# Performance work log

Measured on AMD Instinct MI355X. Metric: run time of the kernel, lower is better.

Reference implementation:

```python
import jax, jax.numpy as jnp
import numpy as np

U_NODES, V_NODES, N_EDGES = 100000, 50000, 2000000
F_DIM, G_DIM, H_DIM = 32, 32, 8
G_HIDDEN = (64, 32)
F_HIDDEN = (64, 32)
OUT_DIM = 1


def _linear_params(key, din, dout):
    kw, kb = jax.random.split(key)
    lim = 1.0 / np.sqrt(din)
    w = jax.random.uniform(kw, (din, dout), jnp.float32, -lim, lim)
    b = jax.random.uniform(kb, (dout,), jnp.float32, -lim, lim)
    return w, b


def setup_inputs() -> dict:
    key = jax.random.key(0)
    ks = jax.random.split(key, 10)
    u = jax.random.normal(ks[0], (U_NODES, F_DIM), jnp.float32)
    v = jax.random.normal(ks[1], (V_NODES, G_DIM), jnp.float32)
    e_vals = jax.random.normal(ks[2], (N_EDGES, H_DIM), jnp.float32)
    e_src = jax.random.randint(ks[3], (N_EDGES,), 0, V_NODES, jnp.int32)  # V-side index (indices[0])
    e_dst = jax.random.randint(ks[4], (N_EDGES,), 0, U_NODES, jnp.int32)  # U-side index (indices[1])
    g_w1, g_b1 = _linear_params(ks[5], F_DIM + G_DIM + H_DIM, G_HIDDEN[0])
    g_w2, g_b2 = _linear_params(ks[6], G_HIDDEN[0], G_HIDDEN[1])
    f_w1, f_b1 = _linear_params(ks[7], F_DIM + G_HIDDEN[1], F_HIDDEN[0])
    f_w2, f_b2 = _linear_params(ks[8], F_HIDDEN[0], F_HIDDEN[1])
    t_w, t_b = _linear_params(ks[9], F_HIDDEN[1], OUT_DIM)
    return {
        "u": u, "v": v, "e_vals": e_vals, "e_src": e_src, "e_dst": e_dst,
        "g_w1": g_w1, "g_b1": g_b1, "g_w2": g_w2, "g_b2": g_b2,
        "f_w1": f_w1, "f_b1": f_b1, "f_w2": f_w2, "f_b2": f_b2,
        "t_w": t_w, "t_b": t_b,
    }


def reference(u, v, e_vals, e_src, e_dst,
              g_w1, g_b1, g_w2, g_b2,
              f_w1, f_b1, f_w2, f_b2,
              t_w, t_b):
    # gather edge endpoint features -> g MLP (two Linear+ReLU layers)
    edge_in = jnp.concatenate([u[e_dst], v[e_src], e_vals], axis=-1)  # (E, F+G+H)
    h = jax.nn.relu(edge_in @ g_w1 + g_b1)
    h = jax.nn.relu(h @ g_w2 + g_b2)  # (E, D)
    # torch.sparse.sum over dim=-3 (V axis) == segment-sum by the U index
    agg = jax.ops.segment_sum(h, e_dst, num_segments=u.shape[0])  # (U, D)
    # f MLP on concat([u, agg])
    z = jax.nn.relu(jnp.concatenate([u, agg], axis=-1) @ f_w1 + f_b1)
    z = jax.nn.relu(z @ f_w2 + f_b2)
    # tail linear (no relu) + sigmoid
    return jax.nn.sigmoid(z @ t_w + t_b)  # (U, 1)
```

## Files before the change

kernel.cpp:

```cpp
#include <hip/hip_runtime.h>
#include <cstdint>
#include <cstddef>

#define U_NODES 100000
#define V_NODES 50000
#define N_EDGES 2000000


typedef _Float16 f16x8 __attribute__((ext_vector_type(8)));
typedef _Float16 f16x2 __attribute__((ext_vector_type(2)));
typedef float    f32x4 __attribute__((ext_vector_type(4)));

__device__ __forceinline__ void load8f(const float* __restrict__ p, float* x) {
    const float4* p4 = reinterpret_cast<const float4*>(p);
    float4 a = p4[0], b = p4[1];
    x[0]=a.x; x[1]=a.y; x[2]=a.z; x[3]=a.w;
    x[4]=b.x; x[5]=b.y; x[6]=b.z; x[7]=b.w;
}

__device__ __forceinline__ void load32f(const float* __restrict__ p, float* x) {
    #pragma unroll
    for (int q = 0; q < 4; ++q) load8f(p + 8*q, x + 8*q);
}

__device__ __forceinline__ unsigned pack_bf16x2(float a, float b) {
    unsigned ua = __float_as_uint(a);
    ua = (ua + 0x7FFFu + ((ua >> 16) & 1u)) >> 16;
    unsigned ub = __float_as_uint(b);
    ub = (ub + 0x7FFFu + ((ub >> 16) & 1u)) & 0xFFFF0000u;
    return ua | ub;
}
__device__ __forceinline__ unsigned short bf16_1(float a) {
    unsigned ua = __float_as_uint(a);
    return (unsigned short)((ua + 0x7FFFu + ((ua >> 16) & 1u)) >> 16);
}

__device__ __forceinline__ unsigned pk16(float a, float b) {
    union { f16x2 h; unsigned u; } c;
    c.h[0] = (_Float16)a; c.h[1] = (_Float16)b;
    return c.u;
}
__device__ __forceinline__ float f16lo(unsigned w) {
    union { unsigned short u; _Float16 h; } c; c.u = (unsigned short)(w & 0xFFFFu);
    return (float)c.h;
}
__device__ __forceinline__ float f16hi(unsigned w) {
    union { unsigned short u; _Float16 h; } c; c.u = (unsigned short)(w >> 16);
    return (float)c.h;
}
__device__ __forceinline__ f16x8 as_f16x8(uint4 x) {
    union { uint4 u; f16x8 h; } c; c.u = x; return c.h;
}

__device__ __forceinline__ float fdot2f(unsigned a, unsigned b, float c) {
#if defined(__has_builtin) && __has_builtin(__builtin_amdgcn_fdot2)
    union { unsigned u; f16x2 h; } ca, cb; ca.u = a; cb.u = b;
    return __builtin_amdgcn_fdot2(ca.h, cb.h, c, false);
#else
    return c + f16lo(a)*f16lo(b) + f16hi(a)*f16hi(b);
#endif
}


__global__ __launch_bounds__(256) void proj_u_kernel(
    const float* __restrict__ u, const float* __restrict__ g_w1,
    float* __restrict__ A)
{
    int n = blockIdx.x * 256 + threadIdx.x;
    if (n >= U_NODES) return;
    float x[32];
    load32f(u + (size_t)n * 32, x);
    float acc[64];
    #pragma unroll
    for (int j = 0; j < 64; ++j) acc[j] = 0.f;
    #pragma unroll
    for (int i = 0; i < 32; ++i) {
        #pragma unroll
        for (int j = 0; j < 64; ++j) acc[j] += x[i] * g_w1[i*64 + j];
    }
    float4* Ap = reinterpret_cast<float4*>(A + (size_t)n * 64);
    #pragma unroll
    for (int q = 0; q < 16; ++q)
        Ap[q] = make_float4(acc[4*q], acc[4*q+1], acc[4*q+2], acc[4*q+3]);
}

__global__ __launch_bounds__(256) void proj_v_kernel(
    const float* __restrict__ v, const float* __restrict__ g_w1,
    const float* __restrict__ g_b1, float* __restrict__ B)
{
    int n = blockIdx.x * 256 + threadIdx.x;
    if (n >= V_NODES) return;
    float x[32];
    load32f(v + (size_t)n * 32, x);
    float acc[64];
    #pragma unroll
    for (int j = 0; j < 64; ++j) acc[j] = g_b1[j];
    #pragma unroll
    for (int i = 0; i < 32; ++i) {
        #pragma unroll
        for (int j = 0; j < 64; ++j) acc[j] += x[i] * g_w1[(32+i)*64 + j];
    }
    float4* Bp = reinterpret_cast<float4*>(B + (size_t)n * 64);
    #pragma unroll
    for (int q = 0; q < 16; ++q)
        Bp[q] = make_float4(acc[4*q], acc[4*q+1], acc[4*q+2], acc[4*q+3]);
}


__global__ __launch_bounds__(256) void rank_kernel(
    const int* __restrict__ e_dst, int* __restrict__ deg, int* __restrict__ rank)
{
    int e = blockIdx.x * 256 + threadIdx.x;
    if (e >= N_EDGES) return;
    rank[e] = atomicAdd(&deg[e_dst[e]], 1);
}

__global__ __launch_bounds__(256) void scan_block_kernel(
    const int* __restrict__ deg, int* __restrict__ off, int* __restrict__ aux, int n)
{
    __shared__ int s[256];
    int tid = threadIdx.x;
    int i = blockIdx.x * 256 + tid;
    int x = (i < n) ? deg[i] : 0;
    s[tid] = x;
    __syncthreads();
    #pragma unroll
    for (int o = 1; o < 256; o <<= 1) {
        int t = (tid >= o) ? s[tid - o] : 0;
        __syncthreads();
        s[tid] += t;
        __syncthreads();
    }
    if (i < n) off[i + 1] = s[tid];
    if (tid == 255) aux[blockIdx.x] = s[255];
}

__global__ __launch_bounds__(512) void scan_aux_kernel(int* __restrict__ aux, int nA)
{
    __shared__ int s[512];
    int tid = threadIdx.x;
    int x = (tid < nA) ? aux[tid] : 0;
    s[tid] = x;
    __syncthreads();
    #pragma unroll
    for (int o = 1; o < 512; o <<= 1) {
        int t = (tid >= o) ? s[tid - o] : 0;
        __syncthreads();
        s[tid] += t;
        __syncthreads();
    }
    if (tid < nA) aux[tid] = s[tid] - x;
}

__global__ __launch_bounds__(256) void scan_add_kernel(
    int* __restrict__ off, const int* __restrict__ aux, int n)
{
    int i = blockIdx.x * 256 + threadIdx.x;
    if (i == 0) off[0] = 0;
    if (i < n) off[i + 1] += aux[i >> 8];
}

__global__ __launch_bounds__(256) void scatter_kernel(
    const int* __restrict__ e_dst, const int* __restrict__ off,
    const int* __restrict__ rank, int* __restrict__ sorted_eid)
{
    int e = blockIdx.x * 256 + threadIdx.x;
    if (e >= N_EDGES) return;
    int d = e_dst[e];
    sorted_eid[off[d] + rank[e]] = e;
}

__global__ __launch_bounds__(256) void permute_pack_kernel(
    const int* __restrict__ e_dst, const int* __restrict__ e_src,
    const int* __restrict__ rank, const int* __restrict__ off,
    const float* __restrict__ e_vals, unsigned* __restrict__ epk)
{
    int e = blockIdx.x * 256 + threadIdx.x;
    if (e >= N_EDGES) return;
    int d = e_dst[e];
    int pos = off[d] + rank[e];
    float ev[8];
    load8f(e_vals + (size_t)e * 8, ev);
    uint4 w0;
    w0.x = (unsigned)d;
    w0.y = (unsigned)e_src[e];
    w0.z = pk16(ev[0], ev[1]);
    w0.w = pk16(ev[2], ev[3]);
    uint2 w1;
    w1.x = pk16(ev[4], ev[5]);
    w1.y = pk16(ev[6], ev[7]);
    unsigned* dst = epk + (size_t)pos * 8;
    *reinterpret_cast<uint4*>(dst)     = w0;
    *reinterpret_cast<uint2*>(dst + 4) = w1;
}


__global__ __launch_bounds__(256) void edge_frag_kernel(
    const float* __restrict__ A, const float* __restrict__ B,
    const unsigned* __restrict__ epk,
    const float* __restrict__ g_w1, const float* __restrict__ g_w2,
    const float* __restrict__ g_b2, float* __restrict__ agg)
{
    __shared__ unsigned s_w2[32 * 33];
    __shared__ __align__(16) unsigned s_w1e[4 * 64];
    __shared__ unsigned s_h2[256 * 17];
    __shared__ int s_d[256];
    __shared__ int s_heads[256];
    __shared__ int s_cnt, s_prevd, s_nextd;

    const int tid = threadIdx.x;
    const long bP = (long)blockIdx.x * 256;

    #pragma unroll
    for (int i = 0; i < 4; ++i) {
        int idx = tid + i * 256;
        int kp = idx >> 5, n = idx & 31;
        s_w2[kp * 33 + n] = pk16(g_w2[(2*kp)*32 + n], g_w2[(2*kp+1)*32 + n]);
    }
    {
        int i2 = tid >> 6, c = tid & 63;
        s_w1e[i2 * 64 + c] = pk16(g_w1[(64 + 2*i2)*64 + c], g_w1[(64 + 2*i2 + 1)*64 + c]);
    }
    if (tid == 0) {
        s_cnt = 0;
        s_prevd = (bP > 0) ? (int)epk[(size_t)(bP - 1) * 8] : -2;
        s_nextd = (bP + 256 < (long)N_EDGES) ? (int)epk[(size_t)(bP + 256) * 8] : -2;
    }

    const int wv   = tid >> 6;
    const int lane = tid & 63;
    const int lm   = lane & 15;
    const int lg   = lane >> 4;
    const long wP  = bP + wv * 64;

    int dM[4], sM[4];
    unsigned evp[4][4];
    #pragma unroll
    for (int mt = 0; mt < 4; ++mt) {
        long pe = wP + mt*16 + lm;
        if (pe < (long)N_EDGES) {
            const unsigned* ep = epk + (size_t)pe * 8;
            uint4 w0 = *reinterpret_cast<const uint4*>(ep);
            uint2 w1 = *reinterpret_cast<const uint2*>(ep + 4);
            dM[mt] = (int)w0.x; sM[mt] = (int)w0.y;
            evp[mt][0] = w0.z; evp[mt][1] = w0.w; evp[mt][2] = w1.x; evp[mt][3] = w1.y;
        } else {
            dM[mt] = -1; sM[mt] = 0;
            evp[mt][0] = evp[mt][1] = evp[mt][2] = evp[mt][3] = 0;
        }
        if (lg == 0) s_d[wv*64 + mt*16 + lm] = dM[mt];
    }
    __syncthreads();

    if (bP + tid < (long)N_EDGES) {
        int d_me  = s_d[tid];
        int prevd = (tid == 0) ? s_prevd : s_d[tid - 1];
        bool true_head = (prevd != d_me);
        bool is_head = (tid == 0) || true_head;
        if (is_head) {
            int idx = atomicAdd(&s_cnt, 1);
            s_heads[idx] = tid | (true_head ? 0x10000 : 0);
        }
    }

    uint4 afr[4][2];
    #pragma unroll
    for (int kt = 0; kt < 2; ++kt) {
        float acc[4][8];
        #pragma unroll
        for (int mt = 0; mt < 4; ++mt) {
            if (dM[mt] >= 0) {
                const float4* Ap = reinterpret_cast<const float4*>(A + (size_t)dM[mt]*64 + kt*32 + lg*8);
                const float4* Bp = reinterpret_cast<const float4*>(B + (size_t)sM[mt]*64 + kt*32 + lg*8);
                float4 a0 = Ap[0], a1 = Ap[1], b0 = Bp[0], b1 = Bp[1];
                acc[mt][0] = a0.x + b0.x; acc[mt][1] = a0.y + b0.y;
                acc[mt][2] = a0.z + b0.z; acc[mt][3] = a0.w + b0.w;
                acc[mt][4] = a1.x + b1.x; acc[mt][5] = a1.y + b1.y;
                acc[mt][6] = a1.z + b1.z; acc[mt][7] = a1.w + b1.w;
            } else {
                #pragma unroll
                for (int j = 0; j < 8; ++j) acc[mt][j] = 0.f;
            }
        }
        #pragma unroll
        for (int i2 = 0; i2 < 4; ++i2) {
            uint4 wA = *reinterpret_cast<const uint4*>(&s_w1e[i2*64 + kt*32 + lg*8]);
            uint4 wB = *reinterpret_cast<const uint4*>(&s_w1e[i2*64 + kt*32 + lg*8 + 4]);
            #pragma unroll
            for (int mt = 0; mt < 4; ++mt) {
                unsigned e2 = evp[mt][i2];
                acc[mt][0] = fdot2f(e2, wA.x, acc[mt][0]);
                acc[mt][1] = fdot2f(e2, wA.y, acc[mt][1]);
                acc[mt][2] = fdot2f(e2, wA.z, acc[mt][2]);
                acc[mt][3] = fdot2f(e2, wA.w, acc[mt][3]);
                acc[mt][4] = fdot2f(e2, wB.x, acc[mt][4]);
                acc[mt][5] = fdot2f(e2, wB.y, acc[mt][5]);
                acc[mt][6] = fdot2f(e2, wB.z, acc[mt][6]);
                acc[mt][7] = fdot2f(e2, wB.w, acc[mt][7]);
            }
        }
        #pragma unroll
        for (int mt = 0; mt < 4; ++mt) {
            uint4 w;
            w.x = pk16(fmaxf(acc[mt][0], 0.f), fmaxf(acc[mt][1], 0.f));
            w.y = pk16(fmaxf(acc[mt][2], 0.f), fmaxf(acc[mt][3], 0.f));
            w.z = pk16(fmaxf(acc[mt][4], 0.f), fmaxf(acc[mt][5], 0.f));
            w.w = pk16(fmaxf(acc[mt][6], 0.f), fmaxf(acc[mt][7], 0.f));
            afr[mt][kt] = w;
        }
    }

    f32x4 mac[4][2];
    #pragma unroll
    for (int mt = 0; mt < 4; ++mt) {
        #pragma unroll
        for (int nt = 0; nt < 2; ++nt) {
            mac[mt][nt][0] = 0.f; mac[mt][nt][1] = 0.f;
            mac[mt][nt][2] = 0.f; mac[mt][nt][3] = 0.f;
        }
    }
    #pragma unroll
    for (int kt = 0; kt < 2; ++kt) {
        uint4 bf0, bf1;
        int kp = kt*16 + lg*4;
        bf0.x = s_w2[(kp+0)*33 + lm];      bf1.x = s_w2[(kp+0)*33 + 16 + lm];
        bf0.y = s_w2[(kp+1)*33 + lm];      bf1.y = s_w2[(kp+1)*33 + 16 + lm];
        bf0.z = s_w2[(kp+2)*33 + lm];      bf1.z = s_w2[(kp+2)*33 + 16 + lm];
        bf0.w = s_w2[(kp+3)*33 + lm];      bf1.w = s_w2[(kp+3)*33 + 16 + lm];
        f16x8 b0 = as_f16x8(bf0), b1 = as_f16x8(bf1);
        #pragma unroll
        for (int mt = 0; mt < 4; ++mt) {
            f16x8 a = as_f16x8(afr[mt][kt]);
            mac[mt][0] = __builtin_amdgcn_mfma_f32_16x16x32_f16(a, b0, mac[mt][0], 0, 0, 0);
            mac[mt][1] = __builtin_amdgcn_mfma_f32_16x16x32_f16(a, b1, mac[mt][1], 0, 0, 0);
        }
    }

    float b2a = g_b2[lm], b2b = g_b2[16 + lm];
    unsigned short* h2s = reinterpret_cast<unsigned short*>(s_h2);
    #pragma unroll
    for (int mt = 0; mt < 4; ++mt) {
        #pragma unroll
        for (int r = 0; r < 4; ++r) {
            int edge = wv*64 + mt*16 + lg*4 + r;
            h2s[edge*34 + lm]      = bf16_1(fmaxf(mac[mt][0][r] + b2a, 0.f));
            h2s[edge*34 + 16 + lm] = bf16_1(fmaxf(mac[mt][1][r] + b2b, 0.f));
        }
    }
    __syncthreads();

    const int nseg = s_cnt;
    const int next_d = s_nextd;
    for (int w = tid; w < nseg * 16; w += 256) {
        int seg = w >> 4, cp = w & 15;
        int ent = s_heads[seg];
        int h = ent & 0xFFFF;
        bool thead = (ent & 0x10000) != 0;
        int dd = s_d[h];
        float s0 = 0.f, s1 = 0.f;
        int r = h;
        while (r < 256 && s_d[r] == dd) {
            unsigned x = s_h2[r*17 + cp];
            s0 += __uint_as_float(x << 16);
            s1 += __uint_as_float(x & 0xFFFF0000u);
            ++r;
        }
        bool end_complete = (r < 256) || (next_d != dd);
        float* dst = agg + (size_t)dd * 32 + 2 * cp;
        if (thead && end_complete) {
            *reinterpret_cast<float2*>(dst) = make_float2(s0, s1);
        } else {
            atomicAdd(dst + 0, s0);
            atomicAdd(dst + 1, s1);
        }
    }
}


template <bool HAS_A>
__global__ __launch_bounds__(256) void edge_mfma_kernel(
    const float* __restrict__ A, const float* __restrict__ B,
    const float* __restrict__ u, const unsigned* __restrict__ epk,
    const float* __restrict__ g_w1, const float* __restrict__ g_w2,
    const float* __restrict__ g_b2, float* __restrict__ agg)
{
    __shared__ unsigned s_h1[256 * 36];
    __shared__ unsigned s_w2[32 * 33];
    __shared__ int s_d[256];
    __shared__ int s_heads[256];
    __shared__ int s_cnt, s_prevd, s_nextd;

    const int tid = threadIdx.x;
    const long p = (long)blockIdx.x * 256 + tid;

    if (tid == 0) {
        s_cnt = 0;
        long pprev = (long)blockIdx.x * 256 - 1;
        s_prevd = (pprev < 0) ? -2 : (int)epk[(size_t)pprev * 8];
        long pnext = (long)blockIdx.x * 256 + 256;
        s_nextd = (pnext >= N_EDGES) ? -2 : (int)epk[(size_t)pnext * 8];
    }
    #pragma unroll
    for (int i = 0; i < 4; ++i) {
        int idx = tid + i * 256;
        int kp = idx >> 5, n = idx & 31;
        s_w2[kp * 33 + n] = pk16(g_w2[(2*kp)*32 + n], g_w2[(2*kp+1)*32 + n]);
    }

    int d = -1;
    if (p < N_EDGES) {
        const unsigned* ep = epk + (size_t)p * 8;
        uint4 w0 = *reinterpret_cast<const uint4*>(ep);
        uint2 w1 = *reinterpret_cast<const uint2*>(ep + 4);
        d = (int)w0.x;
        int s = (int)w0.y;

        float h1[64];
        if constexpr (HAS_A) {
            const float4* Ap = reinterpret_cast<const float4*>(A + (size_t)d * 64);
            #pragma unroll
            for (int q = 0; q < 16; ++q) {
                float4 a = Ap[q];
                h1[4*q+0] = a.x; h1[4*q+1] = a.y; h1[4*q+2] = a.z; h1[4*q+3] = a.w;
            }
        } else {
            #pragma unroll
            for (int j = 0; j < 64; ++j) h1[j] = 0.f;
            float x[32];
            load32f(u + (size_t)d * 32, x);
            #pragma unroll
            for (int i = 0; i < 32; ++i) {
                #pragma unroll
                for (int j = 0; j < 64; ++j) h1[j] += x[i] * g_w1[i*64 + j];
            }
        }
        {
            const float4* Bp = reinterpret_cast<const float4*>(B + (size_t)s * 64);
            #pragma unroll
            for (int q = 0; q < 16; ++q) {
                float4 b = Bp[q];
                h1[4*q+0] += b.x; h1[4*q+1] += b.y; h1[4*q+2] += b.z; h1[4*q+3] += b.w;
            }
        }
        float ev[8];
        ev[0]=f16lo(w0.z); ev[1]=f16hi(w0.z); ev[2]=f16lo(w0.w); ev[3]=f16hi(w0.w);
        ev[4]=f16lo(w1.x); ev[5]=f16hi(w1.x); ev[6]=f16lo(w1.y); ev[7]=f16hi(w1.y);
        #pragma unroll
        for (int i = 0; i < 8; ++i) {
            #pragma unroll
            for (int j = 0; j < 64; ++j) h1[j] += ev[i] * g_w1[(64+i)*64 + j];
        }
        #pragma unroll
        for (int j = 0; j < 64; ++j) h1[j] = fmaxf(h1[j], 0.f);

        #pragma unroll
        for (int q = 0; q < 8; ++q) {
            uint4 w;
            w.x = pk16(h1[8*q+0], h1[8*q+1]);
            w.y = pk16(h1[8*q+2], h1[8*q+3]);
            w.z = pk16(h1[8*q+4], h1[8*q+5]);
            w.w = pk16(h1[8*q+6], h1[8*q+7]);
            *reinterpret_cast<uint4*>(&s_h1[tid*36 + 4*q]) = w;
        }
    }
    s_d[tid] = d;
    __syncthreads();

    if (p < N_EDGES) {
        int prevd = (tid == 0) ? s_prevd : s_d[tid - 1];
        bool true_head = (prevd != d);
        bool is_head = (tid == 0) || true_head;
        if (is_head) {
            int idx = atomicAdd(&s_cnt, 1);
            s_heads[idx] = tid | (true_head ? 0x10000 : 0);
        }
    }

    const int lane = tid & 63;
    const int wb   = (tid >> 6) * 64;
    const int lg   = lane >> 4;
    const int lm   = lane & 15;

    f32x4 acc[4][2];
    #pragma unroll
    for (int mt = 0; mt < 4; ++mt) {
        #pragma unroll
        for (int nt = 0; nt < 2; ++nt) {
            acc[mt][nt][0] = 0.f; acc[mt][nt][1] = 0.f;
            acc[mt][nt][2] = 0.f; acc[mt][nt][3] = 0.f;
        }
    }
    #pragma unroll
    for (int kt = 0; kt < 2; ++kt) {
        uint4 bf0, bf1;
        int kp = kt*16 + lg*4;
        bf0.x = s_w2[(kp+0)*33 + lm];      bf1.x = s_w2[(kp+0)*33 + 16 + lm];
        bf0.y = s_w2[(kp+1)*33 + lm];      bf1.y = s_w2[(kp+1)*33 + 16 + lm];
        bf0.z = s_w2[(kp+2)*33 + lm];      bf1.z = s_w2[(kp+2)*33 + 16 + lm];
        bf0.w = s_w2[(kp+3)*33 + lm];      bf1.w = s_w2[(kp+3)*33 + 16 + lm];
        f16x8 b0 = as_f16x8(bf0), b1 = as_f16x8(bf1);
        #pragma unroll
        for (int mt = 0; mt < 4; ++mt) {
            uint4 av = *reinterpret_cast<const uint4*>(
                &s_h1[(wb + mt*16 + lm)*36 + kt*16 + lg*4]);
            f16x8 a = as_f16x8(av);
            acc[mt][0] = __builtin_amdgcn_mfma_f32_16x16x32_f16(a, b0, acc[mt][0], 0, 0, 0);
            acc[mt][1] = __builtin_amdgcn_mfma_f32_16x16x32_f16(a, b1, acc[mt][1], 0, 0, 0);
        }
    }
    float b2a = g_b2[lm];
    float b2b = g_b2[16 + lm];
    __syncthreads();

    float* h2f = reinterpret_cast<float*>(s_h1);
    #pragma unroll
    for (int mt = 0; mt < 4; ++mt) {
        #pragma unroll
        for (int r = 0; r < 4; ++r) {
            int row = wb + mt*16 + lg*4 + r;
            h2f[row*36 + lm]      = fmaxf(acc[mt][0][r] + b2a, 0.f);
            h2f[row*36 + 16 + lm] = fmaxf(acc[mt][1][r] + b2b, 0.f);
        }
    }
    __syncthreads();

    const int nseg = s_cnt;
    const int next_d = s_nextd;
    for (int w = tid; w < nseg * 16; w += 256) {
        int seg = w >> 4, cp = w & 15;
        int ent = s_heads[seg];
        int h = ent & 0xFFFF;
        bool thead = (ent & 0x10000) != 0;
        int dd = s_d[h];
        float s0 = 0.f, s1 = 0.f;
        int r = h;
        while (r < 256 && s_d[r] == dd) {
            s0 += h2f[r*36 + 2*cp];
            s1 += h2f[r*36 + 2*cp + 1];
            ++r;
        }
        bool end_complete = (r < 256) || (next_d != dd);
        float* dst = agg + (size_t)dd * 32 + 2 * cp;
        if (thead && end_complete) {
            *reinterpret_cast<float2*>(dst) = make_float2(s0, s1);
        } else {
            atomicAdd(dst + 0, s0);
            atomicAdd(dst + 1, s1);
        }
    }
}


template <bool HAS_A, bool HAS_B>
__global__ __launch_bounds__(256) void edge_sorted_kernel(
    const float* __restrict__ A, const float* __restrict__ B,
    const float* __restrict__ u, const float* __restrict__ v,
    const float* __restrict__ e_vals, const int* __restrict__ e_src,
    const int* __restrict__ e_dst, const int* __restrict__ seid,
    const float* __restrict__ g_w1, const float* __restrict__ g_b1,
    const float* __restrict__ g_w2, const float* __restrict__ g_b2,
    float* __restrict__ agg)
{
    __shared__ unsigned lds_h[256][17];
    __shared__ int lds_d[256];
    __shared__ int lds_heads[256];
    __shared__ int lds_cnt;
    __shared__ int lds_prev_d, lds_next_d;

    const int tid = threadIdx.x;
    const long p = (long)blockIdx.x * 256 + tid;

    if (tid == 0) {
        lds_cnt = 0;
        long pprev = (long)blockIdx.x * 256 - 1;
        lds_prev_d = (pprev < 0) ? -2 : e_dst[seid[pprev]];
        long pnext = (long)blockIdx.x * 256 + 256;
        lds_next_d = (pnext >= N_EDGES) ? -2 : e_dst[seid[pnext]];
    }

    int d = -1;
    if (p < N_EDGES) {
        int eid = seid[p];
        d = e_dst[eid];
        int s = e_src[eid];

        float h1[64];
        if constexpr (HAS_A) {
            const float4* Ap = reinterpret_cast<const float4*>(A + (size_t)d * 64);
            #pragma unroll
            for (int q = 0; q < 16; ++q) {
                float4 a = Ap[q];
                h1[4*q+0] = a.x; h1[4*q+1] = a.y; h1[4*q+2] = a.z; h1[4*q+3] = a.w;
            }
        } else {
            #pragma unroll
            for (int j = 0; j < 64; ++j) h1[j] = 0.f;
            float x[32];
            load32f(u + (size_t)d * 32, x);
            #pragma unroll
            for (int i = 0; i < 32; ++i) {
                #pragma unroll
                for (int j = 0; j < 64; ++j) h1[j] += x[i] * g_w1[i*64 + j];
            }
        }
        if constexpr (HAS_B) {
            const float4* Bp = reinterpret_cast<const float4*>(B + (size_t)s * 64);
            #pragma unroll
            for (int q = 0; q < 16; ++q) {
                float4 b = Bp[q];
                h1[4*q+0] += b.x; h1[4*q+1] += b.y; h1[4*q+2] += b.z; h1[4*q+3] += b.w;
            }
        } else {
            #pragma unroll
            for (int j = 0; j < 64; ++j) h1[j] += g_b1[j];
            float x[32];
            load32f(v + (size_t)s * 32, x);
            #pragma unroll
            for (int i = 0; i < 32; ++i) {
                #pragma unroll
                for (int j = 0; j < 64; ++j) h1[j] += x[i] * g_w1[(32+i)*64 + j];
            }
        }
        float ev[8];
        load8f(e_vals + (size_t)eid * 8, ev);
        #pragma unroll
        for (int i = 0; i < 8; ++i) {
            #pragma unroll
            for (int j = 0; j < 64; ++j) h1[j] += ev[i] * g_w1[(64+i)*64 + j];
        }
        #pragma unroll
        for (int j = 0; j < 64; ++j) h1[j] = fmaxf(h1[j], 0.f);

        float h2[32];
        #pragma unroll
        for (int k = 0; k < 32; ++k) h2[k] = g_b2[k];
        #pragma unroll
        for (int i = 0; i < 64; ++i) {
            #pragma unroll
            for (int k = 0; k < 32; ++k) h2[k] += h1[i] * g_w2[i*32 + k];
        }
        #pragma unroll
        for (int cp = 0; cp < 16; ++cp)
            lds_h[tid][cp] = pack_bf16x2(fmaxf(h2[2*cp], 0.f), fmaxf(h2[2*cp+1], 0.f));
    }
    lds_d[tid] = d;
    __syncthreads();

    if (p < N_EDGES) {
        int prevd = (tid == 0) ? lds_prev_d : lds_d[tid - 1];
        bool true_head = (prevd != d);
        bool is_head = (tid == 0) || true_head;
        if (is_head) {
            int idx = atomicAdd(&lds_cnt, 1);
            lds_heads[idx] = tid | (true_head ? 0x10000 : 0);
        }
    }
    __syncthreads();

    const int nseg = lds_cnt;
    const int next_d = lds_next_d;
    for (int w = tid; w < nseg * 16; w += 256) {
        int seg = w >> 4, cp = w & 15;
        int ent = lds_heads[seg];
        int h = ent & 0xFFFF;
        bool thead = (ent & 0x10000) != 0;
        int dd = lds_d[h];
        float s0 = 0.f, s1 = 0.f;
        int r = h;
        while (r < 256 && lds_d[r] == dd) {
            unsigned x = lds_h[r][cp];
            s0 += __uint_as_float(x << 16);
            s1 += __uint_as_float(x & 0xFFFF0000u);
            ++r;
        }
        bool end_complete = (r < 256) || (next_d != dd);
        float* dst = agg + (size_t)dd * 32 + 2 * cp;
        if (thead && end_complete) {
            *reinterpret_cast<float2*>(dst) = make_float2(s0, s1);
        } else {
            atomicAdd(dst + 0, s0);
            atomicAdd(dst + 1, s1);
        }
    }
}


__global__ __launch_bounds__(256) void node_kernel(
    const float* __restrict__ u, const float* __restrict__ agg,
    const float* __restrict__ f_w1, const float* __restrict__ f_b1,
    const float* __restrict__ f_w2, const float* __restrict__ f_b2,
    const float* __restrict__ t_w, const float* __restrict__ t_b,
    float* __restrict__ out)
{
    int n = blockIdx.x * 256 + threadIdx.x;
    if (n >= U_NODES) return;
    float x[64];
    load32f(u   + (size_t)n * 32, x);
    load32f(agg + (size_t)n * 32, x + 32);
    float z1[64];
    #pragma unroll
    for (int j = 0; j < 64; ++j) z1[j] = f_b1[j];
    #pragma unroll
    for (int i = 0; i < 64; ++i) {
        #pragma unroll
        for (int j = 0; j < 64; ++j) z1[j] += x[i] * f_w1[i*64 + j];
    }
    #pragma unroll
    for (int j = 0; j < 64; ++j) z1[j] = fmaxf(z1[j], 0.f);
    float z2[32];
    #pragma unroll
    for (int k = 0; k < 32; ++k) z2[k] = f_b2[k];
    #pragma unroll
    for (int j = 0; j < 64; ++j) {
        #pragma unroll
        for (int k = 0; k < 32; ++k) z2[k] += z1[j] * f_w2[j*32 + k];
    }
    #pragma unroll
    for (int k = 0; k < 32; ++k) z2[k] = fmaxf(z2[k], 0.f);
    float o = t_b[0];
    #pragma unroll
    for (int k = 0; k < 32; ++k) o += z2[k] * t_w[k];
    out[n] = 1.f / (1.f + expf(-o));
}


__global__ __launch_bounds__(256) void edge_direct_kernel(
    const float* __restrict__ u, const float* __restrict__ v,
    const float* __restrict__ e_vals, const int* __restrict__ e_src,
    const int* __restrict__ e_dst, const float* __restrict__ g_w1,
    const float* __restrict__ g_b1, const float* __restrict__ g_w2,
    const float* __restrict__ g_b2, float* __restrict__ agg)
{
    int e = blockIdx.x * 256 + threadIdx.x;
    if (e >= N_EDGES) return;
    int d = e_dst[e];
    int s = e_src[e];
    float x[72];
    load32f(u + (size_t)d * 32, x);
    load32f(v + (size_t)s * 32, x + 32);
    load8f(e_vals + (size_t)e * 8, x + 64);
    float h1[64];
    #pragma unroll
    for (int j = 0; j < 64; ++j) h1[j] = g_b1[j];
    #pragma unroll
    for (int i = 0; i < 72; ++i) {
        #pragma unroll
        for (int j = 0; j < 64; ++j) h1[j] += x[i] * g_w1[i*64 + j];
    }
    #pragma unroll
    for (int j = 0; j < 64; ++j) h1[j] = fmaxf(h1[j], 0.f);
    float acc2[32];
    #pragma unroll
    for (int k = 0; k < 32; ++k) acc2[k] = g_b2[k];
    #pragma unroll
    for (int i = 0; i < 64; ++i) {
        #pragma unroll
        for (int k = 0; k < 32; ++k) acc2[k] += h1[i] * g_w2[i*32 + k];
    }
    float* aggp = agg + (size_t)d * 32;
    #pragma unroll
    for (int k = 0; k < 32; ++k) atomicAdd(aggp + k, fmaxf(acc2[k], 0.f));
}


static inline size_t align256(size_t x) { return (x + 255) & ~(size_t)255; }

extern "C" void kernel_launch(void* const* d_in, const int* in_sizes, int n_in,
                              void* d_out, int out_size, void* d_ws, size_t ws_size,
                              hipStream_t stream) {
    const float* u      = (const float*)d_in[0];
    const float* v      = (const float*)d_in[1];
    const float* e_vals = (const float*)d_in[2];
    const int*   e_src  = (const int*)  d_in[3];
    const int*   e_dst  = (const int*)  d_in[4];
    const float* g_w1   = (const float*)d_in[5];
    const float* g_b1   = (const float*)d_in[6];
    const float* g_w2   = (const float*)d_in[7];
    const float* g_b2   = (const float*)d_in[8];
    const float* f_w1   = (const float*)d_in[9];
    const float* f_b1   = (const float*)d_in[10];
    const float* f_w2   = (const float*)d_in[11];
    const float* f_b2   = (const float*)d_in[12];
    const float* t_w    = (const float*)d_in[13];
    const float* t_b    = (const float*)d_in[14];
    float* out = (float*)d_out;

    char* wsc = (char*)d_ws;
    const int nChunks = (U_NODES + 255) / 256;
    const int eBlocks = (N_EDGES + 255) / 256;

    const size_t degB  = align256((size_t)U_NODES * 4);
    const size_t offB  = align256((size_t)(U_NODES + 1) * 4);
    const size_t auxB  = align256((size_t)nChunks * 4);
    const size_t aggB  = align256((size_t)U_NODES * 32 * 4);
    const size_t e4B   = align256((size_t)N_EDGES * 4);
    const size_t epkB  = align256((size_t)N_EDGES * 32);
    const size_t bB    = align256((size_t)V_NODES * 64 * 4);
    const size_t aB    = align256((size_t)U_NODES * 64 * 4);

    size_t o = 0;
    size_t oDeg = o; o += degB;
    size_t oOff = o; o += offB;
    size_t oAux = o; o += auxB;
    size_t oAgg = o; o += aggB;
    size_t baseNeed = o;

    size_t oEp = o;  o += epkB;
    size_t oBn = o;  o += bB;
    size_t needT2r = o + e4B;
    size_t oAn = o;  o += aB;
    size_t needT1 = o;

    size_t o3 = baseNeed;
    size_t oSeid = o3; o3 += e4B;
    size_t needT4 = o3 + e4B;
    size_t oB3 = o3;   o3 += bB;
    size_t oA3 = o3;   o3 += aB;
    size_t needT3 = o3;

    int* deg   = (int*)(wsc + oDeg);
    int* off   = (int*)(wsc + oOff);
    int* aux   = (int*)(wsc + oAux);
    float* agg = (float*)(wsc + oAgg);

    if (ws_size >= needT2r) {
        const bool hasA = (ws_size >= needT1);
        unsigned* epk = (unsigned*)(wsc + oEp);
        float* B   = (float*)(wsc + oBn);
        float* A   = hasA ? (float*)(wsc + oAn) : nullptr;
        int* rank  = hasA ? (int*)A : (int*)(wsc + oAn);

        hipMemsetAsync(deg, 0, (size_t)U_NODES * 4, stream);
        hipMemsetAsync(agg, 0, (size_t)U_NODES * 32 * 4, stream);

        rank_kernel<<<eBlocks, 256, 0, stream>>>(e_dst, deg, rank);
        scan_block_kernel<<<nChunks, 256, 0, stream>>>(deg, off, aux, U_NODES);
        scan_aux_kernel<<<1, 512, 0, stream>>>(aux, nChunks);
        scan_add_kernel<<<nChunks, 256, 0, stream>>>(off, aux, U_NODES);
        permute_pack_kernel<<<eBlocks, 256, 0, stream>>>(e_dst, e_src, rank, off,
                                                         e_vals, epk);
        proj_v_kernel<<<(V_NODES + 255) / 256, 256, 0, stream>>>(v, g_w1, g_b1, B);
        if (hasA) {
            proj_u_kernel<<<(U_NODES + 255) / 256, 256, 0, stream>>>(u, g_w1, A);
            edge_frag_kernel<<<eBlocks, 256, 0, stream>>>(
                A, B, epk, g_w1, g_w2, g_b2, agg);
        } else {
            edge_mfma_kernel<false><<<eBlocks, 256, 0, stream>>>(
                nullptr, B, u, epk, g_w1, g_w2, g_b2, agg);
        }
        node_kernel<<<(U_NODES + 255) / 256, 256, 0, stream>>>(
            u, agg, f_w1, f_b1, f_w2, f_b2, t_w, t_b, out);
    } else if (ws_size >= needT4) {
        const bool hasAB = (ws_size >= needT3);
        int* seid = (int*)(wsc + oSeid);
        float* B = hasAB ? (float*)(wsc + oB3) : nullptr;
        float* A = hasAB ? (float*)(wsc + oA3) : nullptr;
        int* rank = hasAB ? (int*)A : (int*)(wsc + oSeid + e4B);

        hipMemsetAsync(deg, 0, (size_t)U_NODES * 4, stream);
        hipMemsetAsync(agg, 0, (size_t)U_NODES * 32 * 4, stream);

        rank_kernel<<<eBlocks, 256, 0, stream>>>(e_dst, deg, rank);
        scan_block_kernel<<<nChunks, 256, 0, stream>>>(deg, off, aux, U_NODES);
        scan_aux_kernel<<<1, 512, 0, stream>>>(aux, nChunks);
        scan_add_kernel<<<nChunks, 256, 0, stream>>>(off, aux, U_NODES);
        scatter_kernel<<<eBlocks, 256, 0, stream>>>(e_dst, off, rank, seid);

        if (hasAB) {
            proj_v_kernel<<<(V_NODES + 255) / 256, 256, 0, stream>>>(v, g_w1, g_b1, B);
            proj_u_kernel<<<(U_NODES + 255) / 256, 256, 0, stream>>>(u, g_w1, A);
            edge_sorted_kernel<true, true><<<eBlocks, 256, 0, stream>>>(
                A, B, u, v, e_vals, e_src, e_dst, seid, g_w1, g_b1, g_w2, g_b2, agg);
        } else {
            edge_sorted_kernel<false, false><<<eBlocks, 256, 0, stream>>>(
                nullptr, nullptr, u, v, e_vals, e_src, e_dst, seid,
                g_w1, g_b1, g_w2, g_b2, agg);
        }
        node_kernel<<<(U_NODES + 255) / 256, 256, 0, stream>>>(
            u, agg, f_w1, f_b1, f_w2, f_b2, t_w, t_b, out);
    } else {
        float* agg0 = (float*)wsc;
        hipMemsetAsync(agg0, 0, (size_t)U_NODES * 32 * 4, stream);
        edge_direct_kernel<<<eBlocks, 256, 0, stream>>>(
            u, v, e_vals, e_src, e_dst, g_w1, g_b1, g_w2, g_b2, agg0);
        node_kernel<<<(U_NODES + 255) / 256, 256, 0, stream>>>(
            u, agg0, f_w1, f_b1, f_w2, f_b2, t_w, t_b, out);
    }
}
```

Measured before the change: 424.4 us.

## Make edge kernel persistent with double-buffered tiles and merge U/V projections

Replaces the one-tile-per-block edge kernel with a persistent grid-stride kernel of up to 768 blocks. Each block prefetches the next tile's packed edge records and runs the previous tile's segment reduction and atomics while computing the current tile's MLP, using double-buffered shared memory. The U and V projection kernels are also merged into one launch. The aim is to hide gather latency and save launch and weight-staging overhead per tile. The cost is more shared memory and registers per block and fewer blocks in flight.

```diff
diff --git a/kernel.cpp b/kernel.cpp
--- a/kernel.cpp
+++ b/kernel.cpp
@@ -5,6 +5,8 @@
 #define U_NODES 100000
 #define V_NODES 50000
 #define N_EDGES 2000000
+#define UBLKS ((U_NODES + 255) / 256)
+#define VBLKS ((V_NODES + 255) / 256)
 
 
 typedef _Float16 f16x8 __attribute__((ext_vector_type(8)));
@@ -104,6 +106,48 @@
     #pragma unroll
     for (int q = 0; q < 16; ++q)
         Bp[q] = make_float4(acc[4*q], acc[4*q+1], acc[4*q+2], acc[4*q+3]);
+}
+
+__global__ __launch_bounds__(256) void proj_uv_kernel(
+    const float* __restrict__ u, const float* __restrict__ v,
+    const float* __restrict__ g_w1, const float* __restrict__ g_b1,
+    float* __restrict__ A, float* __restrict__ B)
+{
+    if (blockIdx.x < UBLKS) {
+        int n = blockIdx.x * 256 + threadIdx.x;
+        if (n >= U_NODES) return;
+        float x[32];
+        load32f(u + (size_t)n * 32, x);
+        float acc[64];
+        #pragma unroll
+        for (int j = 0; j < 64; ++j) acc[j] = 0.f;
+        #pragma unroll
+        for (int i = 0; i < 32; ++i) {
+            #pragma unroll
+            for (int j = 0; j < 64; ++j) acc[j] += x[i] * g_w1[i*64 + j];
+        }
+        float4* Ap = reinterpret_cast<float4*>(A + (size_t)n * 64);
+        #pragma unroll
+        for (int q = 0; q < 16; ++q)
+            Ap[q] = make_float4(acc[4*q], acc[4*q+1], acc[4*q+2], acc[4*q+3]);
+    } else {
+        int n = (blockIdx.x - UBLKS) * 256 + threadIdx.x;
+        if (n >= V_NODES) return;
+        float x[32];
+        load32f(v + (size_t)n * 32, x);
+        float acc[64];
+        #pragma unroll
+        for (int j = 0; j < 64; ++j) acc[j] = g_b1[j];
+        #pragma unroll
+        for (int i = 0; i < 32; ++i) {
+            #pragma unroll
+            for (int j = 0; j < 64; ++j) acc[j] += x[i] * g_w1[(32+i)*64 + j];
+        }
+        float4* Bp = reinterpret_cast<float4*>(B + (size_t)n * 64);
+        #pragma unroll
+        for (int q = 0; q < 16; ++q)
+            Bp[q] = make_float4(acc[4*q], acc[4*q+1], acc[4*q+2], acc[4*q+3]);
+    }
 }
 
 
@@ -195,49 +239,13 @@
 }
 
 
-__global__ __launch_bounds__(256) void edge_frag_kernel(
-    const float* __restrict__ A, const float* __restrict__ B,
-    const unsigned* __restrict__ epk,
-    const float* __restrict__ g_w1, const float* __restrict__ g_w2,
-    const float* __restrict__ g_b2, float* __restrict__ agg)
-{
-    __shared__ unsigned s_w2[32 * 33];
-    __shared__ __align__(16) unsigned s_w1e[4 * 64];
-    __shared__ unsigned s_h2[256 * 17];
-    __shared__ int s_d[256];
-    __shared__ int s_heads[256];
-    __shared__ int s_cnt, s_prevd, s_nextd;
-
-    const int tid = threadIdx.x;
-    const long bP = (long)blockIdx.x * 256;
-
-    #pragma unroll
-    for (int i = 0; i < 4; ++i) {
-        int idx = tid + i * 256;
-        int kp = idx >> 5, n = idx & 31;
-        s_w2[kp * 33 + n] = pk16(g_w2[(2*kp)*32 + n], g_w2[(2*kp+1)*32 + n]);
-    }
-    {
-        int i2 = tid >> 6, c = tid & 63;
-        s_w1e[i2 * 64 + c] = pk16(g_w1[(64 + 2*i2)*64 + c], g_w1[(64 + 2*i2 + 1)*64 + c]);
-    }
-    if (tid == 0) {
-        s_cnt = 0;
-        s_prevd = (bP > 0) ? (int)epk[(size_t)(bP - 1) * 8] : -2;
-        s_nextd = (bP + 256 < (long)N_EDGES) ? (int)epk[(size_t)(bP + 256) * 8] : -2;
-    }
-
-    const int wv   = tid >> 6;
-    const int lane = tid & 63;
-    const int lm   = lane & 15;
-    const int lg   = lane >> 4;
-    const long wP  = bP + wv * 64;
-
-    int dM[4], sM[4];
-    unsigned evp[4][4];
+__device__ __forceinline__ void load_recs(
+    const unsigned* __restrict__ epk, long base, int wv, int lm,
+    int* dM, int* sM, unsigned (*evp)[4])
+{
     #pragma unroll
     for (int mt = 0; mt < 4; ++mt) {
-        long pe = wP + mt*16 + lm;
+        long pe = base + wv*64 + mt*16 + lm;
         if (pe < (long)N_EDGES) {
             const unsigned* ep = epk + (size_t)pe * 8;
             uint4 w0 = *reinterpret_cast<const uint4*>(ep);
@@ -248,119 +256,24 @@
             dM[mt] = -1; sM[mt] = 0;
             evp[mt][0] = evp[mt][1] = evp[mt][2] = evp[mt][3] = 0;
         }
-        if (lg == 0) s_d[wv*64 + mt*16 + lm] = dM[mt];
-    }
-    __syncthreads();
-
-    if (bP + tid < (long)N_EDGES) {
-        int d_me  = s_d[tid];
-        int prevd = (tid == 0) ? s_prevd : s_d[tid - 1];
-        bool true_head = (prevd != d_me);
-        bool is_head = (tid == 0) || true_head;
-        if (is_head) {
-            int idx = atomicAdd(&s_cnt, 1);
-            s_heads[idx] = tid | (true_head ? 0x10000 : 0);
-        }
-    }
-
-    uint4 afr[4][2];
-    #pragma unroll
-    for (int kt = 0; kt < 2; ++kt) {
-        float acc[4][8];
-        #pragma unroll
-        for (int mt = 0; mt < 4; ++mt) {
-            if (dM[mt] >= 0) {
-                const float4* Ap = reinterpret_cast<const float4*>(A + (size_t)dM[mt]*64 + kt*32 + lg*8);
-                const float4* Bp = reinterpret_cast<const float4*>(B + (size_t)sM[mt]*64 + kt*32 + lg*8);
-                float4 a0 = Ap[0], a1 = Ap[1], b0 = Bp[0], b1 = Bp[1];
-                acc[mt][0] = a0.x + b0.x; acc[mt][1] = a0.y + b0.y;
-                acc[mt][2] = a0.z + b0.z; acc[mt][3] = a0.w + b0.w;
-                acc[mt][4] = a1.x + b1.x; acc[mt][5] = a1.y + b1.y;
-                acc[mt][6] = a1.z + b1.z; acc[mt][7] = a1.w + b1.w;
-            } else {
-                #pragma unroll
-                for (int j = 0; j < 8; ++j) acc[mt][j] = 0.f;
-            }
-        }
-        #pragma unroll
-        for (int i2 = 0; i2 < 4; ++i2) {
-            uint4 wA = *reinterpret_cast<const uint4*>(&s_w1e[i2*64 + kt*32 + lg*8]);
-            uint4 wB = *reinterpret_cast<const uint4*>(&s_w1e[i2*64 + kt*32 + lg*8 + 4]);
-            #pragma unroll
-            for (int mt = 0; mt < 4; ++mt) {
-                unsigned e2 = evp[mt][i2];
-                acc[mt][0] = fdot2f(e2, wA.x, acc[mt][0]);
-                acc[mt][1] = fdot2f(e2, wA.y, acc[mt][1]);
-                acc[mt][2] = fdot2f(e2, wA.z, acc[mt][2]);
-                acc[mt][3] = fdot2f(e2, wA.w, acc[mt][3]);
-                acc[mt][4] = fdot2f(e2, wB.x, acc[mt][4]);
-                acc[mt][5] = fdot2f(e2, wB.y, acc[mt][5]);
-                acc[mt][6] = fdot2f(e2, wB.z, acc[mt][6]);
-                acc[mt][7] = fdot2f(e2, wB.w, acc[mt][7]);
-            }
-        }
-        #pragma unroll
-        for (int mt = 0; mt < 4; ++mt) {
-            uint4 w;
-            w.x = pk16(fmaxf(acc[mt][0], 0.f), fmaxf(acc[mt][1], 0.f));
-            w.y = pk16(fmaxf(acc[mt][2], 0.f), fmaxf(acc[mt][3], 0.f));
-            w.z = pk16(fmaxf(acc[mt][4], 0.f), fmaxf(acc[mt][5], 0.f));
-            w.w = pk16(fmaxf(acc[mt][6], 0.f), fmaxf(acc[mt][7], 0.f));
-            afr[mt][kt] = w;
-        }
-    }
-
-    f32x4 mac[4][2];
-    #pragma unroll
-    for (int mt = 0; mt < 4; ++mt) {
-        #pragma unroll
-        for (int nt = 0; nt < 2; ++nt) {
-            mac[mt][nt][0] = 0.f; mac[mt][nt][1] = 0.f;
-            mac[mt][nt][2] = 0.f; mac[mt][nt][3] = 0.f;
-        }
-    }
-    #pragma unroll
-    for (int kt = 0; kt < 2; ++kt) {
-        uint4 bf0, bf1;
-        int kp = kt*16 + lg*4;
-        bf0.x = s_w2[(kp+0)*33 + lm];      bf1.x = s_w2[(kp+0)*33 + 16 + lm];
-        bf0.y = s_w2[(kp+1)*33 + lm];      bf1.y = s_w2[(kp+1)*33 + 16 + lm];
-        bf0.z = s_w2[(kp+2)*33 + lm];      bf1.z = s_w2[(kp+2)*33 + 16 + lm];
-        bf0.w = s_w2[(kp+3)*33 + lm];      bf1.w = s_w2[(kp+3)*33 + 16 + lm];
-        f16x8 b0 = as_f16x8(bf0), b1 = as_f16x8(bf1);
-        #pragma unroll
-        for (int mt = 0; mt < 4; ++mt) {
-            f16x8 a = as_f16x8(afr[mt][kt]);
-            mac[mt][0] = __builtin_amdgcn_mfma_f32_16x16x32_f16(a, b0, mac[mt][0], 0, 0, 0);
-            mac[mt][1] = __builtin_amdgcn_mfma_f32_16x16x32_f16(a, b1, mac[mt][1], 0, 0, 0);
-        }
-    }
-
-    float b2a = g_b2[lm], b2b = g_b2[16 + lm];
-    unsigned short* h2s = reinterpret_cast<unsigned short*>(s_h2);
-    #pragma unroll
-    for (int mt = 0; mt < 4; ++mt) {
-        #pragma unroll
-        for (int r = 0; r < 4; ++r) {
-            int edge = wv*64 + mt*16 + lg*4 + r;
-            h2s[edge*34 + lm]      = bf16_1(fmaxf(mac[mt][0][r] + b2a, 0.f));
-            h2s[edge*34 + 16 + lm] = bf16_1(fmaxf(mac[mt][1][r] + b2b, 0.f));
-        }
-    }
-    __syncthreads();
-
-    const int nseg = s_cnt;
-    const int next_d = s_nextd;
+    }
+}
+
+__device__ __forceinline__ void seg_reduce_256(
+    const unsigned* __restrict__ h2b, const int* __restrict__ db,
+    const int* __restrict__ headsb, int nseg, int next_d,
+    int tid, float* __restrict__ agg)
+{
     for (int w = tid; w < nseg * 16; w += 256) {
         int seg = w >> 4, cp = w & 15;
-        int ent = s_heads[seg];
+        int ent = headsb[seg];
         int h = ent & 0xFFFF;
         bool thead = (ent & 0x10000) != 0;
-        int dd = s_d[h];
+        int dd = db[h];
         float s0 = 0.f, s1 = 0.f;
         int r = h;
-        while (r < 256 && s_d[r] == dd) {
-            unsigned x = s_h2[r*17 + cp];
+        while (r < 256 && db[r] == dd) {
+            unsigned x = h2b[r*17 + cp];
             s0 += __uint_as_float(x << 16);
             s1 += __uint_as_float(x & 0xFFFF0000u);
             ++r;
@@ -374,6 +287,192 @@
             atomicAdd(dst + 1, s1);
         }
     }
+}
+
+
+__global__ __launch_bounds__(256, 4) void edge_pipe_kernel(
+    const float* __restrict__ A, const float* __restrict__ B,
+    const unsigned* __restrict__ epk,
+    const float* __restrict__ g_w1, const float* __restrict__ g_w2,
+    const float* __restrict__ g_b2, float* __restrict__ agg,
+    int nTiles, int stride)
+{
+    __shared__ unsigned s_w2[32 * 33];
+    __shared__ __align__(16) unsigned s_w1e[4 * 64];
+    __shared__ unsigned s_h2[2][256 * 17];
+    __shared__ int s_d[2][256];
+    __shared__ int s_heads[2][256];
+    __shared__ int s_cnt[2];
+    __shared__ int s_bprev[2], s_bnext[2];
+
+    const int tid = threadIdx.x;
+
+    #pragma unroll
+    for (int i = 0; i < 4; ++i) {
+        int idx = tid + i * 256;
+        int kp = idx >> 5, n = idx & 31;
+        s_w2[kp * 33 + n] = pk16(g_w2[(2*kp)*32 + n], g_w2[(2*kp+1)*32 + n]);
+    }
+    {
+        int i2 = tid >> 6, c = tid & 63;
+        s_w1e[i2 * 64 + c] = pk16(g_w1[(64 + 2*i2)*64 + c], g_w1[(64 + 2*i2 + 1)*64 + c]);
+    }
+
+    const int wv   = tid >> 6;
+    const int lane = tid & 63;
+    const int lm   = lane & 15;
+    const int lg   = lane >> 4;
+    const float b2a = g_b2[lm], b2b = g_b2[16 + lm];
+
+    int tile = blockIdx.x;
+    if (tile >= nTiles) return;
+
+    int dC[4], sC[4]; unsigned evC[4][4];
+    load_recs(epk, (long)tile * 256, wv, lm, dC, sC, evC);
+
+    __syncthreads();
+
+    int ct = 0;
+    bool hasPend = false;
+    while (true) {
+        const long bP = (long)tile * 256;
+        const int ntile = tile + stride;
+
+        int dN[4], sN[4]; unsigned evN[4][4];
+        if (ntile < nTiles) {
+            load_recs(epk, (long)ntile * 256, wv, lm, dN, sN, evN);
+        } else {
+            #pragma unroll
+            for (int mt = 0; mt < 4; ++mt) {
+                dN[mt] = -1; sN[mt] = 0;
+                evN[mt][0] = evN[mt][1] = evN[mt][2] = evN[mt][3] = 0;
+            }
+        }
+        if (tid == 0) {
+            s_cnt[ct] = 0;
+            s_bprev[ct] = (bP > 0) ? (int)epk[(size_t)(bP - 1) * 8] : -2;
+            s_bnext[ct] = (bP + 256 < (long)N_EDGES) ? (int)epk[(size_t)(bP + 256) * 8] : -2;
+        }
+
+        if (hasPend) {
+            seg_reduce_256(s_h2[ct ^ 1], s_d[ct ^ 1], s_heads[ct ^ 1],
+                           s_cnt[ct ^ 1], s_bnext[ct ^ 1], tid, agg);
+        }
+
+        if (lg == 0) {
+            #pragma unroll
+            for (int mt = 0; mt < 4; ++mt) s_d[ct][wv*64 + mt*16 + lm] = dC[mt];
+        }
+
+        uint4 afr[4][2];
+        #pragma unroll
+        for (int kt = 0; kt < 2; ++kt) {
+            float acc[4][8];
+            #pragma unroll
+            for (int mt = 0; mt < 4; ++mt) {
+                if (dC[mt] >= 0) {
+                    const float4* Ap = reinterpret_cast<const float4*>(A + (size_t)dC[mt]*64 + kt*32 + lg*8);
+                    const float4* Bp = reinterpret_cast<const float4*>(B + (size_t)sC[mt]*64 + kt*32 + lg*8);
+                    float4 a0 = Ap[0], a1 = Ap[1], b0 = Bp[0], b1 = Bp[1];
+                    acc[mt][0] = a0.x + b0.x; acc[mt][1] = a0.y + b0.y;
+                    acc[mt][2] = a0.z + b0.z; acc[mt][3] = a0.w + b0.w;
+                    acc[mt][4] = a1.x + b1.x; acc[mt][5] = a1.y + b1.y;
+                    acc[mt][6] = a1.z + b1.z; acc[mt][7] = a1.w + b1.w;
+                } else {
+                    #pragma unroll
+                    for (int j = 0; j < 8; ++j) acc[mt][j] = 0.f;
+                }
+            }
+            #pragma unroll
+            for (int i2 = 0; i2 < 4; ++i2) {
+                uint4 wA = *reinterpret_cast<const uint4*>(&s_w1e[i2*64 + kt*32 + lg*8]);
+                uint4 wB = *reinterpret_cast<const uint4*>(&s_w1e[i2*64 + kt*32 + lg*8 + 4]);
+                #pragma unroll
+                for (int mt = 0; mt < 4; ++mt) {
+                    unsigned e2 = evC[mt][i2];
+                    acc[mt][0] = fdot2f(e2, wA.x, acc[mt][0]);
+                    acc[mt][1] = fdot2f(e2, wA.y, acc[mt][1]);
+                    acc[mt][2] = fdot2f(e2, wA.z, acc[mt][2]);
+                    acc[mt][3] = fdot2f(e2, wA.w, acc[mt][3]);
+                    acc[mt][4] = fdot2f(e2, wB.x, acc[mt][4]);
+                    acc[mt][5] = fdot2f(e2, wB.y, acc[mt][5]);
+                    acc[mt][6] = fdot2f(e2, wB.z, acc[mt][6]);
+                    acc[mt][7] = fdot2f(e2, wB.w, acc[mt][7]);
+                }
+            }
+            #pragma unroll
+            for (int mt = 0; mt < 4; ++mt) {
+                uint4 w;
+                w.x = pk16(fmaxf(acc[mt][0], 0.f), fmaxf(acc[mt][1], 0.f));
+                w.y = pk16(fmaxf(acc[mt][2], 0.f), fmaxf(acc[mt][3], 0.f));
+                w.z = pk16(fmaxf(acc[mt][4], 0.f), fmaxf(acc[mt][5], 0.f));
+                w.w = pk16(fmaxf(acc[mt][6], 0.f), fmaxf(acc[mt][7], 0.f));
+                afr[mt][kt] = w;
+            }
+        }
+
+        f32x4 mac[4][2];
+        #pragma unroll
+        for (int mt = 0; mt < 4; ++mt) {
+            #pragma unroll
+            for (int nt = 0; nt < 2; ++nt) {
+                mac[mt][nt][0] = 0.f; mac[mt][nt][1] = 0.f;
+                mac[mt][nt][2] = 0.f; mac[mt][nt][3] = 0.f;
+            }
+        }
+        #pragma unroll
+        for (int kt = 0; kt < 2; ++kt) {
+            uint4 bf0, bf1;
+            int kp = kt*16 + lg*4;
+            bf0.x = s_w2[(kp+0)*33 + lm];      bf1.x = s_w2[(kp+0)*33 + 16 + lm];
+            bf0.y = s_w2[(kp+1)*33 + lm];      bf1.y = s_w2[(kp+1)*33 + 16 + lm];
+            bf0.z = s_w2[(kp+2)*33 + lm];      bf1.z = s_w2[(kp+2)*33 + 16 + lm];
+            bf0.w = s_w2[(kp+3)*33 + lm];      bf1.w = s_w2[(kp+3)*33 + 16 + lm];
+            f16x8 b0 = as_f16x8(bf0), b1 = as_f16x8(bf1);
+            #pragma unroll
+            for (int mt = 0; mt < 4; ++mt) {
+                f16x8 a = as_f16x8(afr[mt][kt]);
+                mac[mt][0] = __builtin_amdgcn_mfma_f32_16x16x32_f16(a, b0, mac[mt][0], 0, 0, 0);
+                mac[mt][1] = __builtin_amdgcn_mfma_f32_16x16x32_f16(a, b1, mac[mt][1], 0, 0, 0);
+            }
+        }
+
+        unsigned short* h2s = reinterpret_cast<unsigned short*>(s_h2[ct]);
+        #pragma unroll
+        for (int mt = 0; mt < 4; ++mt) {
+            #pragma unroll
+            for (int r = 0; r < 4; ++r) {
+                int edge = wv*64 + mt*16 + lg*4 + r;
+                h2s[edge*34 + lm]      = bf16_1(fmaxf(mac[mt][0][r] + b2a, 0.f));
+                h2s[edge*34 + 16 + lm] = bf16_1(fmaxf(mac[mt][1][r] + b2b, 0.f));
+            }
+        }
+        __syncthreads();
+
+        if (bP + tid < (long)N_EDGES) {
+            int dme  = s_d[ct][tid];
+            int prevd = (tid == 0) ? s_bprev[ct] : s_d[ct][tid - 1];
+            bool th = (prevd != dme);
+            bool ih = (tid == 0) || th;
+            if (ih) {
+                int idx = atomicAdd(&s_cnt[ct], 1);
+                s_heads[ct][idx] = tid | (th ? 0x10000 : 0);
+            }
+        }
+        __syncthreads();
+
+        hasPend = true;
+        if (ntile >= nTiles) break;
+        #pragma unroll
+        for (int mt = 0; mt < 4; ++mt) {
+            dC[mt] = dN[mt]; sC[mt] = sN[mt];
+            evC[mt][0] = evN[mt][0]; evC[mt][1] = evN[mt][1];
+            evC[mt][2] = evN[mt][2]; evC[mt][3] = evN[mt][3];
+        }
+        tile = ntile; ct ^= 1;
+    }
+
+    seg_reduce_256(s_h2[ct], s_d[ct], s_heads[ct], s_cnt[ct], s_bnext[ct], tid, agg);
 }
 
 
@@ -839,12 +938,14 @@
         scan_add_kernel<<<nChunks, 256, 0, stream>>>(off, aux, U_NODES);
         permute_pack_kernel<<<eBlocks, 256, 0, stream>>>(e_dst, e_src, rank, off,
                                                          e_vals, epk);
-        proj_v_kernel<<<(V_NODES + 255) / 256, 256, 0, stream>>>(v, g_w1, g_b1, B);
         if (hasA) {
-            proj_u_kernel<<<(U_NODES + 255) / 256, 256, 0, stream>>>(u, g_w1, A);
-            edge_frag_kernel<<<eBlocks, 256, 0, stream>>>(
-                A, B, epk, g_w1, g_w2, g_b2, agg);
+            proj_uv_kernel<<<UBLKS + VBLKS, 256, 0, stream>>>(u, v, g_w1, g_b1, A, B);
+            int nTiles = eBlocks;
+            int gblk = 768 < nTiles ? 768 : nTiles;
+            edge_pipe_kernel<<<gblk, 256, 0, stream>>>(
+                A, B, epk, g_w1, g_w2, g_b2, agg, nTiles, gblk);
         } else {
+            proj_v_kernel<<<VBLKS, 256, 0, stream>>>(v, g_w1, g_b1, B);
             edge_mfma_kernel<false><<<eBlocks, 256, 0, stream>>>(
                 nullptr, B, u, epk, g_w1, g_w2, g_b2, agg);
         }
@@ -867,8 +968,8 @@
         scatter_kernel<<<eBlocks, 256, 0, stream>>>(e_dst, off, rank, seid);
 
         if (hasAB) {
-            proj_v_kernel<<<(V_NODES + 255) / 256, 256, 0, stream>>>(v, g_w1, g_b1, B);
-            proj_u_kernel<<<(U_NODES + 255) / 256, 256, 0, stream>>>(u, g_w1, A);
+            proj_v_kernel<<<VBLKS, 256, 0, stream>>>(v, g_w1, g_b1, B);
+            proj_u_kernel<<<UBLKS, 256, 0, stream>>>(u, g_w1, A);
             edge_sorted_kernel<true, true><<<eBlocks, 256, 0, stream>>>(
                 A, B, u, v, e_vals, e_src, e_dst, seid, g_w1, g_b1, g_w2, g_b2, agg);
         } else {
```

Result: slower. 1.142 ms (+169.0%).
